# Optimization experiments

Measured on AMD Instinct MI355X. Metric: run time of the kernel, lower is better.

## Reference

```python
import jax, jax.numpy as jnp
import numpy as np

N_NODES = 100000
HIDDEN = 64
N_LAYERS = 4
N_EDGES = 800000
EPS = 1e-5  # equinox RMSNorm default


def rmsnorm(x, w):
    # per-node RMSNorm over last dim, learned scale, no bias
    inv = jax.lax.rsqrt(jnp.mean(x * x, axis=-1, keepdims=True) + EPS)
    return x * inv * w


def setup_inputs() -> dict:
    key = jax.random.key(0)
    ks = jax.random.split(key, 5)
    x = jax.random.normal(ks[0], (N_NODES, HIDDEN), dtype=jnp.float32)
    # eqx Linear weight (out,in), init ~ U(-1/sqrt(in), 1/sqrt(in)); randn*scale is fine for a baseline
    scale = 1.0 / np.sqrt(HIDDEN)
    conv_w = jax.random.normal(ks[1], (N_LAYERS, HIDDEN, HIDDEN), dtype=jnp.float32) * scale
    hid_w = jax.random.normal(ks[2], (N_LAYERS, HIDDEN, HIDDEN), dtype=jnp.float32) * scale
    conv_norm_w = jnp.ones((N_LAYERS, HIDDEN), dtype=jnp.float32)
    hid_norm_w = jnp.ones((N_LAYERS, HIDDEN), dtype=jnp.float32)
    row = jax.random.randint(ks[3], (N_EDGES,), 0, N_NODES, dtype=jnp.int32)
    col = jax.random.randint(ks[4], (N_EDGES,), 0, N_NODES, dtype=jnp.int32)
    return {"x": x, "conv_w": conv_w, "conv_norm_w": conv_norm_w,
            "hid_w": hid_w, "hid_norm_w": hid_norm_w, "row": row, "col": col}


def reference(x, conv_w, conv_norm_w, hid_w, hid_norm_w, row, col):
    n_nodes = x.shape[0]

    def step(h, params):
        cw, cnw, hw, hnw = params
        # GConvLayer: linear (no bias) -> relu -> sparse adjacency aggregation -> residual RMSNorm
        m = jax.nn.relu(h @ cw.T)                                  # [n_nodes, d]
        agg = jax.ops.segment_sum(m[col], row, num_segments=n_nodes)  # a @ m (unweighted COO)
        h = rmsnorm(h + agg, cnw)
        # HiddenLayer: linear -> relu -> residual RMSNorm
        y = jax.nn.relu(h @ hw.T)
        h = rmsnorm(h + y, hnw)
        return h, None

    x, _ = jax.lax.scan(step, x, (conv_w, conv_norm_w, hid_w, hid_norm_w))
    return x
```

## Files before the change

### kernel.cpp

```cpp
#include <hip/hip_runtime.h>
#include <hip/hip_bf16.h>

#define HIDDEN 64
#define EPS 1e-5f
#define NPB 64
#define FNPB 32
#define WST 72

typedef __attribute__((ext_vector_type(8))) short bf16x8;
typedef __attribute__((ext_vector_type(4))) float f32x4;

__device__ __forceinline__ unsigned short f2b(float x) {
    __hip_bfloat16 b = __float2bfloat16(x);
    return *(unsigned short*)&b;
}
__device__ __forceinline__ float b2f(unsigned short u) {
    unsigned int ui = (unsigned int)u << 16;
    return *(float*)&ui;
}
__device__ __forceinline__ float b2f_lo(unsigned int u) { unsigned int ui = u << 16; return *(float*)&ui; }
__device__ __forceinline__ float b2f_hi(unsigned int u) { unsigned int ui = u & 0xffff0000u; return *(float*)&ui; }
__device__ __forceinline__ unsigned int pk2(float a, float b) {
    return (unsigned int)f2b(a) | ((unsigned int)f2b(b) << 16);
}


__global__ __launch_bounds__(256) void hist_rank_kernel(const int* __restrict__ row,
                                                        int* __restrict__ cnt,
                                                        int* __restrict__ erank, int e) {
    int stride = gridDim.x * blockDim.x;
    for (int i = blockIdx.x * blockDim.x + threadIdx.x; i < e; i += stride) {
        int r = row[i];
        erank[i] = atomicAdd(&cnt[r], 1);
    }
}

__global__ __launch_bounds__(256) void block_sum_kernel(const int* __restrict__ cnt,
                                                        int* __restrict__ bsum, int n) {
    __shared__ int wsum[4];
    int tid = threadIdx.x;
    int i = blockIdx.x * 256 + tid;
    int v = (i < n) ? cnt[i] : 0;
#pragma unroll
    for (int off = 32; off > 0; off >>= 1) v += __shfl_xor(v, off, 64);
    if ((tid & 63) == 0) wsum[tid >> 6] = v;
    __syncthreads();
    if (tid == 0) bsum[blockIdx.x] = wsum[0] + wsum[1] + wsum[2] + wsum[3];
}

__global__ __launch_bounds__(256) void scan_final_kernel(const int* __restrict__ cnt,
                                                         const int* __restrict__ bsum,
                                                         int* __restrict__ row_ptr,
                                                         int n, int nb) {
    __shared__ int wred[4];
    __shared__ int wsum[4];
    __shared__ int wexcl[4];
    __shared__ int s_prev;
    __shared__ int s_tot;
    int b = blockIdx.x;
    int tid = threadIdx.x;
    int lane = tid & 63;
    int w = tid >> 6;
    int acc = 0;
    for (int j = tid; j < b; j += 256) acc += bsum[j];
#pragma unroll
    for (int off = 32; off > 0; off >>= 1) acc += __shfl_xor(acc, off, 64);
    if (lane == 0) wred[w] = acc;
    int i = b * 256 + tid;
    int v = (i < n) ? cnt[i] : 0;
    int sc = v;
#pragma unroll
    for (int off = 1; off < 64; off <<= 1) {
        int t = __shfl_up(sc, off, 64);
        if (lane >= off) sc += t;
    }
    if (lane == 63) wsum[w] = sc;
    __syncthreads();
    if (tid == 0) {
        s_prev = wred[0] + wred[1] + wred[2] + wred[3];
        int a = 0;
#pragma unroll
        for (int j = 0; j < 4; j++) { wexcl[j] = a; a += wsum[j]; }
        s_tot = a;
    }
    __syncthreads();
    if (i < n) row_ptr[i] = s_prev + wexcl[w] + (sc - v);
    if (b == nb - 1 && tid == 0) row_ptr[n] = s_prev + s_tot;
}

__global__ __launch_bounds__(256) void fill_kernel(const int* __restrict__ row,
                                                   const int* __restrict__ col,
                                                   const int* __restrict__ row_ptr,
                                                   const int* __restrict__ erank,
                                                   int* __restrict__ ecol, int e, int n) {
    int cls = blockIdx.x & 7;
    int sub = blockIdx.x >> 3;
    int nsub = gridDim.x >> 3;
    int lo = (int)(((long long)n * cls) >> 3);
    int hi = (int)(((long long)n * (cls + 1)) >> 3);
    for (int i = sub * 256 + threadIdx.x; i < e; i += nsub * 256) {
        int r = row[i];
        if (r >= lo && r < hi) {
            int pos = row_ptr[r] + erank[i];
            ecol[pos] = col[i];
        }
    }
}

__global__ __launch_bounds__(256) void wconv_kernel(const float* __restrict__ cw,
                                                    const float* __restrict__ hw,
                                                    unsigned short* __restrict__ wbt,
                                                    unsigned short* __restrict__ mA,
                                                    unsigned short* __restrict__ mB,
                                                    int L, int n) {
    int idx = blockIdx.x * blockDim.x + threadIdx.x;
    int total = 2 * L * 4096;
    if (idx < total) {
        int mat = idx >> 12;
        int rem = idx & 4095;
        const float* src = (mat < L) ? (cw + (size_t)mat * 4096) : (hw + (size_t)(mat - L) * 4096);
        wbt[idx] = f2b(src[rem]);
    } else if (idx < total + HIDDEN) {
        int k = idx - total;
        mA[(size_t)n * HIDDEN + k] = 0;
        mB[(size_t)n * HIDDEN + k] = 0;
    }
}


__device__ __forceinline__ void mfma_tile(const unsigned short* s_a,
                                          const unsigned short* s_b,
                                          int l16, int quad, int wbase, f32x4 acc[4]) {
    const unsigned short* ap = &s_a[(size_t)(wbase + l16) * WST + quad * 8];
    const unsigned short* bp = &s_b[(size_t)l16 * WST + quad * 8];
#pragma unroll
    for (int kt = 0; kt < 2; kt++) {
        bf16x8 a = *(const bf16x8*)(ap + kt * 32);
#pragma unroll
        for (int nt = 0; nt < 4; nt++) {
            bf16x8 b = *(const bf16x8*)(bp + (size_t)nt * 16 * WST + kt * 32);
            acc[nt] = __builtin_amdgcn_mfma_f32_16x16x32_bf16(a, b, acc[nt], 0, 0, 0);
        }
    }
}

__device__ __forceinline__ void load_wfrag(const unsigned short* __restrict__ w,
                                           int l16, int quad, bf16x8 wf[8]) {
    const unsigned short* wp = w + (size_t)l16 * 64 + quad * 8;
#pragma unroll
    for (int nt = 0; nt < 4; nt++) {
#pragma unroll
        for (int kt = 0; kt < 2; kt++)
            wf[nt * 2 + kt] = *(const bf16x8*)(wp + (size_t)nt * 16 * 64 + kt * 32);
    }
}

__device__ __forceinline__ void stage_wb(const unsigned short* __restrict__ wsrc,
                                         unsigned short* s_wb, int tid) {
    for (int i = tid; i < 512; i += 256) {
        int r = i >> 3, seg = i & 7;
        *(uint4*)(&s_wb[r * WST + seg * 8]) = ((const uint4*)(wsrc + r * 64))[seg];
    }
}

__device__ __forceinline__ void acc8(float* p, uint4 u) {
    p[0] += b2f_lo(u.x);
    p[1] += b2f_hi(u.x);
    p[2] += b2f_lo(u.y);
    p[3] += b2f_hi(u.y);
    p[4] += b2f_lo(u.z);
    p[5] += b2f_hi(u.z);
    p[6] += b2f_lo(u.w);
    p[7] += b2f_hi(u.w);
}


__global__ __launch_bounds__(256) void mm_relu_kernel(const float* __restrict__ h,
                                                      const unsigned short* __restrict__ wb,
                                                      __hip_bfloat16* __restrict__ m, int n) {
    __shared__ unsigned short s_hb[NPB * WST];
    __shared__ unsigned short s_wb[64 * WST];
    int tid = threadIdx.x;
    int base = blockIdx.x * NPB;
    stage_wb(wb, s_wb, tid);
    for (int i = tid; i < 512; i += 256) {
        int r = i >> 3, seg = i & 7;
        if (base + r < n) {
            const float4* hp = (const float4*)(h + (size_t)(base + r) * HIDDEN + seg * 8);
            float4 ha = hp[0], hb = hp[1];
            uint4 p;
            p.x = pk2(ha.x, ha.y);
            p.y = pk2(ha.z, ha.w);
            p.z = pk2(hb.x, hb.y);
            p.w = pk2(hb.z, hb.w);
            *(uint4*)(&s_hb[r * WST + seg * 8]) = p;
        } else {
            *(uint4*)(&s_hb[r * WST + seg * 8]) = make_uint4(0u, 0u, 0u, 0u);
        }
    }
    __syncthreads();
    int lane = tid & 63, wave = tid >> 6;
    int quad = lane >> 4, l16 = lane & 15;
    int wbase = wave * 16;
    f32x4 acc[4];
    acc[0] = (f32x4){0.f,0.f,0.f,0.f}; acc[1] = (f32x4){0.f,0.f,0.f,0.f};
    acc[2] = (f32x4){0.f,0.f,0.f,0.f}; acc[3] = (f32x4){0.f,0.f,0.f,0.f};
    mfma_tile(s_hb, s_wb, l16, quad, wbase, acc);
    unsigned short* mo = (unsigned short*)m;
#pragma unroll
    for (int r = 0; r < 4; r++) {
        int node = base + wbase + quad * 4 + r;
        if (node < n) {
#pragma unroll
            for (int nt = 0; nt < 4; nt++)
                mo[(size_t)node * HIDDEN + nt * 16 + l16] = f2b(fmaxf(acc[nt][r], 0.f));
        }
    }
}


__global__ __launch_bounds__(128, 6) void fused_layer_kernel(
        const float* hf, const __hip_bfloat16* hb_in,
        const __hip_bfloat16* __restrict__ m_in,
        const unsigned short* __restrict__ hwb,
        const unsigned short* cwb_next,
        const int* __restrict__ row_ptr, const int* __restrict__ ecol,
        const float* __restrict__ cnw, const float* __restrict__ hnw,
        float* out_f32, __hip_bfloat16* hb_new, __hip_bfloat16* m_out, int n) {
    __shared__ unsigned short s_hb[FNPB * WST];
    int tid = threadIdx.x;
    int base = blockIdx.x * FNPB;
    int lane = tid & 63, wave = tid >> 6;

    int g = lane >> 2;
    int sl = lane & 3;
    int gb = lane & ~3;
    int nl = wave * 16 + g;
    int node = base + nl;

    const unsigned short* mi = (const unsigned short*)m_in;

    uint4 q0 = make_uint4(0u, 0u, 0u, 0u);
    uint4 q1 = make_uint4(0u, 0u, 0u, 0u);
    if (node < n) {
        float p[16];
        if (hf) {
            const float4* hp = (const float4*)(hf + (size_t)node * HIDDEN + 16 * sl);
            float4 v0 = hp[0], v1 = hp[1], v2 = hp[2], v3 = hp[3];
            p[0]=v0.x;  p[1]=v0.y;  p[2]=v0.z;  p[3]=v0.w;
            p[4]=v1.x;  p[5]=v1.y;  p[6]=v1.z;  p[7]=v1.w;
            p[8]=v2.x;  p[9]=v2.y;  p[10]=v2.z; p[11]=v2.w;
            p[12]=v3.x; p[13]=v3.y; p[14]=v3.z; p[15]=v3.w;
        } else {
            const uint4* hp = (const uint4*)((const unsigned short*)hb_in + (size_t)node * HIDDEN + 16 * sl);
            uint4 u0 = hp[0], u1 = hp[1];
            p[0]=b2f_lo(u0.x);  p[1]=b2f_hi(u0.x);
            p[2]=b2f_lo(u0.y);  p[3]=b2f_hi(u0.y);
            p[4]=b2f_lo(u0.z);  p[5]=b2f_hi(u0.z);
            p[6]=b2f_lo(u0.w);  p[7]=b2f_hi(u0.w);
            p[8]=b2f_lo(u1.x);  p[9]=b2f_hi(u1.x);
            p[10]=b2f_lo(u1.y); p[11]=b2f_hi(u1.y);
            p[12]=b2f_lo(u1.z); p[13]=b2f_hi(u1.z);
            p[14]=b2f_lo(u1.w); p[15]=b2f_hi(u1.w);
        }
        int beg = row_ptr[node];
        int end = row_ptr[node + 1];
        int myc = 0;
        if (beg < end) {
            int idx = beg + sl;
            myc = ecol[idx < end ? idx : end - 1];
        }
        for (int b0 = beg; b0 < end; b0 += 4) {
            int nxt = b0 + 4;
            int nmyc = 0;
            if (nxt < end) {
                int idx = nxt + sl;
                nmyc = ecol[idx < end ? idx : end - 1];
            }
            int cnt = end - b0;
            int cj[4];
#pragma unroll
            for (int j = 0; j < 4; j++) {
                int c = __shfl(myc, gb + j, 64);
                cj[j] = (j < cnt) ? c : n;
            }
            uint4 ua[4], ub[4];
#pragma unroll
            for (int j = 0; j < 4; j++) {
                const uint4* mp = (const uint4*)(mi + (size_t)cj[j] * HIDDEN + 16 * sl);
                ua[j] = mp[0];
                ub[j] = mp[1];
            }
#pragma unroll
            for (int j = 0; j < 4; j++) {
                acc8(p, ua[j]);
                acc8(p + 8, ub[j]);
            }
            myc = nmyc;
        }
        float ss = 0.f;
#pragma unroll
        for (int k = 0; k < 16; k++) ss += p[k] * p[k];
        ss += __shfl_xor(ss, 1, 64);
        ss += __shfl_xor(ss, 2, 64);
        float inv = rsqrtf(ss * (1.0f / 64.0f) + EPS);
        const float4* cp = (const float4*)(cnw + 16 * sl);
        float4 c0 = cp[0], c1 = cp[1], c2 = cp[2], c3 = cp[3];
        q0.x = pk2(p[0]*inv*c0.x,  p[1]*inv*c0.y);
        q0.y = pk2(p[2]*inv*c0.z,  p[3]*inv*c0.w);
        q0.z = pk2(p[4]*inv*c1.x,  p[5]*inv*c1.y);
        q0.w = pk2(p[6]*inv*c1.z,  p[7]*inv*c1.w);
        q1.x = pk2(p[8]*inv*c2.x,  p[9]*inv*c2.y);
        q1.y = pk2(p[10]*inv*c2.z, p[11]*inv*c2.w);
        q1.z = pk2(p[12]*inv*c3.x, p[13]*inv*c3.y);
        q1.w = pk2(p[14]*inv*c3.z, p[15]*inv*c3.w);
    }
    *(uint4*)(&s_hb[(size_t)nl * WST + 16 * sl]) = q0;
    *(uint4*)(&s_hb[(size_t)nl * WST + 16 * sl + 8]) = q1;

    int quad = lane >> 4, l16 = lane & 15;
    int wbase = wave * 16;
    bf16x8 wfh[8];
    load_wfrag(hwb, l16, quad, wfh);
    f32x4 acc[4];
    acc[0] = (f32x4){0.f,0.f,0.f,0.f}; acc[1] = (f32x4){0.f,0.f,0.f,0.f};
    acc[2] = (f32x4){0.f,0.f,0.f,0.f}; acc[3] = (f32x4){0.f,0.f,0.f,0.f};
    {
        const unsigned short* ap = &s_hb[(size_t)(wbase + l16) * WST + quad * 8];
#pragma unroll
        for (int kt = 0; kt < 2; kt++) {
            bf16x8 a = *(const bf16x8*)(ap + kt * 32);
#pragma unroll
            for (int nt = 0; nt < 4; nt++)
                acc[nt] = __builtin_amdgcn_mfma_f32_16x16x32_bf16(a, wfh[nt * 2 + kt], acc[nt], 0, 0, 0);
        }
    }

    float hv[4][4];
    float ssq[4] = {0.f, 0.f, 0.f, 0.f};
#pragma unroll
    for (int r = 0; r < 4; r++) {
        int nr = wbase + quad * 4 + r;
#pragma unroll
        for (int nt = 0; nt < 4; nt++) {
            float hres = b2f(s_hb[(size_t)nr * WST + nt * 16 + l16]);
            float v = hres + fmaxf(acc[nt][r], 0.f);
            hv[r][nt] = v;
            ssq[r] += v * v;
        }
    }
#pragma unroll
    for (int mk = 1; mk <= 8; mk <<= 1) {
#pragma unroll
        for (int r = 0; r < 4; r++) ssq[r] += __shfl_xor(ssq[r], mk, 64);
    }
    bf16x8 wfc[8];
    if (m_out) load_wfrag(cwb_next, l16, quad, wfc);
    float nwv[4];
#pragma unroll
    for (int nt = 0; nt < 4; nt++) nwv[nt] = hnw[nt * 16 + l16];
#pragma unroll
    for (int r = 0; r < 4; r++) {
        float inv = rsqrtf(ssq[r] * (1.0f / 64.0f) + EPS);
#pragma unroll
        for (int nt = 0; nt < 4; nt++) hv[r][nt] *= inv * nwv[nt];
    }
    if (out_f32) {
#pragma unroll
        for (int r = 0; r < 4; r++) {
            int nd = base + wbase + quad * 4 + r;
            if (nd < n) {
#pragma unroll
                for (int nt = 0; nt < 4; nt++)
                    out_f32[(size_t)nd * HIDDEN + nt * 16 + l16] = hv[r][nt];
            }
        }
    }
    if (hb_new) {
        unsigned short* ho = (unsigned short*)hb_new;
#pragma unroll
        for (int r = 0; r < 4; r++) {
            int nd = base + wbase + quad * 4 + r;
            if (nd < n) {
#pragma unroll
                for (int nt = 0; nt < 4; nt++)
                    ho[(size_t)nd * HIDDEN + nt * 16 + l16] = f2b(hv[r][nt]);
            }
        }
    }

    if (!m_out) return;

#pragma unroll
    for (int r = 0; r < 4; r++) {
        int nr = wbase + quad * 4 + r;
#pragma unroll
        for (int nt = 0; nt < 4; nt++)
            s_hb[(size_t)nr * WST + nt * 16 + l16] = f2b(hv[r][nt]);
    }

    f32x4 acc2[4];
    acc2[0] = (f32x4){0.f,0.f,0.f,0.f}; acc2[1] = (f32x4){0.f,0.f,0.f,0.f};
    acc2[2] = (f32x4){0.f,0.f,0.f,0.f}; acc2[3] = (f32x4){0.f,0.f,0.f,0.f};
    {
        const unsigned short* ap = &s_hb[(size_t)(wbase + l16) * WST + quad * 8];
#pragma unroll
        for (int kt = 0; kt < 2; kt++) {
            bf16x8 a = *(const bf16x8*)(ap + kt * 32);
#pragma unroll
            for (int nt = 0; nt < 4; nt++)
                acc2[nt] = __builtin_amdgcn_mfma_f32_16x16x32_bf16(a, wfc[nt * 2 + kt], acc2[nt], 0, 0, 0);
        }
    }
    unsigned short* mo = (unsigned short*)m_out;
#pragma unroll
    for (int r = 0; r < 4; r++) {
        int nd = base + wbase + quad * 4 + r;
        if (nd < n) {
#pragma unroll
            for (int nt = 0; nt < 4; nt++)
                mo[(size_t)nd * HIDDEN + nt * 16 + l16] = f2b(fmaxf(acc2[nt][r], 0.f));
        }
    }
}


static inline size_t align_up(size_t x, size_t a) { return (x + a - 1) & ~(a - 1); }

extern "C" void kernel_launch(void* const* d_in, const int* in_sizes, int n_in,
                              void* d_out, int out_size, void* d_ws, size_t ws_size,
                              hipStream_t stream) {
    const float* x       = (const float*)d_in[0];
    const float* conv_w  = (const float*)d_in[1];
    const float* conv_nw = (const float*)d_in[2];
    const float* hid_w   = (const float*)d_in[3];
    const float* hid_nw  = (const float*)d_in[4];
    const int*   row     = (const int*)d_in[5];
    const int*   col     = (const int*)d_in[6];
    float* out = (float*)d_out;

    const int n = in_sizes[0] / HIDDEN;
    const int e = in_sizes[5];
    const int L = in_sizes[1] / 4096;

    size_t off = 0;
    char* ws = (char*)d_ws;
    __hip_bfloat16* mA = (__hip_bfloat16*)(ws + off);  off = align_up(off + (size_t)(n + 1) * HIDDEN * 2, 16);
    __hip_bfloat16* mB = (__hip_bfloat16*)(ws + off);  off = align_up(off + (size_t)(n + 1) * HIDDEN * 2, 16);
    __hip_bfloat16* hb1 = (__hip_bfloat16*)(ws + off); off = align_up(off + (size_t)n * HIDDEN * 2, 16);
    __hip_bfloat16* hb2 = (__hip_bfloat16*)(ws + off); off = align_up(off + (size_t)n * HIDDEN * 2, 16);
    unsigned short* wbt = (unsigned short*)(ws + off); off = align_up(off + (size_t)2 * L * 4096 * 2, 16);
    int* row_ptr = (int*)(ws + off);           off = align_up(off + (size_t)(n + 1) * 4, 16);
    int* cnt = (int*)(ws + off);               off = align_up(off + (size_t)n * 4, 16);
    int* bsum = (int*)(ws + off);              off = align_up(off + (size_t)1024 * 4, 16);
    int* erank = (int*)(ws + off);             off = align_up(off + (size_t)e * 4, 16);
    int* ecol = (int*)(ws + off);              off = align_up(off + (size_t)e * 4, 16);

    const int nb = (n + 255) / 256;

    hipMemsetAsync(cnt, 0, (size_t)n * 4, stream);
    hist_rank_kernel<<<1024, 256, 0, stream>>>(row, cnt, erank, e);
    block_sum_kernel<<<nb, 256, 0, stream>>>(cnt, bsum, n);
    scan_final_kernel<<<nb, 256, 0, stream>>>(cnt, bsum, row_ptr, n, nb);
    fill_kernel<<<1024, 256, 0, stream>>>(row, col, row_ptr, erank, ecol, e, n);

    wconv_kernel<<<(2 * L * 4096 + HIDDEN + 255) / 256, 256, 0, stream>>>(
        conv_w, hid_w, wbt, (unsigned short*)mA, (unsigned short*)mB, L, n);

    mm_relu_kernel<<<(n + NPB - 1) / NPB, 256, 0, stream>>>(x, wbt, mA, n);

    const int fblocks = (n + FNPB - 1) / FNPB;
    const __hip_bfloat16* mi = mA;
    __hip_bfloat16* mo = mB;
    __hip_bfloat16* hin = nullptr;
    __hip_bfloat16* hout = hb1;
    for (int l = 0; l < L; l++) {
        bool last = (l == L - 1);
        fused_layer_kernel<<<fblocks, 128, 0, stream>>>(
            (l == 0) ? x : nullptr, hin, mi,
            wbt + (size_t)(L + l) * 4096,
            last ? nullptr : (wbt + (size_t)(l + 1) * 4096),
            row_ptr, ecol,
            conv_nw + (size_t)l * HIDDEN, hid_nw + (size_t)l * HIDDEN,
            last ? out : nullptr,
            last ? nullptr : hout,
            last ? nullptr : mo, n);
        __hip_bfloat16* tmp = (__hip_bfloat16*)mi; mi = mo; mo = tmp;
        hin = hout;
        hout = (hout == hb1) ? hb2 : hb1;
    }
}
```

Baseline: 296.6 us.

## Use eight lanes per node in fused layer gather with 256-thread blocks

Each node's gather and RMSNorm is now handled by 8 lanes instead of 4. Each lane loads 16 bytes per neighbor row, and the loop processes 8 edges per iteration, so more independent memory loads are in flight. Blocks grow to 256 threads (4 waves), each wave covering 8 nodes. Each wave's 16-row MFMA tile is now half filled with zero padding, which doubles the matrix work and the wave count per node in exchange for more gather parallelism.

```diff
diff --git a/kernel.cpp b/kernel.cpp
--- a/kernel.cpp
+++ b/kernel.cpp
@@ -219,7 +219,7 @@
 }
 
 
-__global__ __launch_bounds__(128, 6) void fused_layer_kernel(
+__global__ __launch_bounds__(256, 6) void fused_layer_kernel(
         const float* hf, const __hip_bfloat16* hb_in,
         const __hip_bfloat16* __restrict__ m_in,
         const unsigned short* __restrict__ hwb,
@@ -227,41 +227,35 @@
         const int* __restrict__ row_ptr, const int* __restrict__ ecol,
         const float* __restrict__ cnw, const float* __restrict__ hnw,
         float* out_f32, __hip_bfloat16* hb_new, __hip_bfloat16* m_out, int n) {
-    __shared__ unsigned short s_hb[FNPB * WST];
+    __shared__ unsigned short s_hb[64 * WST];
     int tid = threadIdx.x;
     int base = blockIdx.x * FNPB;
     int lane = tid & 63, wave = tid >> 6;
 
-    int g = lane >> 2;
-    int sl = lane & 3;
-    int gb = lane & ~3;
+    int g = lane >> 3;
+    int sl = lane & 7;
+    int gb = lane & ~7;
     int nl = wave * 16 + g;
-    int node = base + nl;
+    int node = base + wave * 8 + g;
+
+    *(uint4*)(&s_hb[(size_t)(wave * 16 + 8 + g) * WST + 8 * sl]) = make_uint4(0u, 0u, 0u, 0u);
 
     const unsigned short* mi = (const unsigned short*)m_in;
 
     uint4 q0 = make_uint4(0u, 0u, 0u, 0u);
-    uint4 q1 = make_uint4(0u, 0u, 0u, 0u);
     if (node < n) {
-        float p[16];
+        float p[8];
         if (hf) {
-            const float4* hp = (const float4*)(hf + (size_t)node * HIDDEN + 16 * sl);
-            float4 v0 = hp[0], v1 = hp[1], v2 = hp[2], v3 = hp[3];
-            p[0]=v0.x;  p[1]=v0.y;  p[2]=v0.z;  p[3]=v0.w;
-            p[4]=v1.x;  p[5]=v1.y;  p[6]=v1.z;  p[7]=v1.w;
-            p[8]=v2.x;  p[9]=v2.y;  p[10]=v2.z; p[11]=v2.w;
-            p[12]=v3.x; p[13]=v3.y; p[14]=v3.z; p[15]=v3.w;
+            const float4* hp = (const float4*)(hf + (size_t)node * HIDDEN + 8 * sl);
+            float4 v0 = hp[0], v1 = hp[1];
+            p[0]=v0.x; p[1]=v0.y; p[2]=v0.z; p[3]=v0.w;
+            p[4]=v1.x; p[5]=v1.y; p[6]=v1.z; p[7]=v1.w;
         } else {
-            const uint4* hp = (const uint4*)((const unsigned short*)hb_in + (size_t)node * HIDDEN + 16 * sl);
-            uint4 u0 = hp[0], u1 = hp[1];
-            p[0]=b2f_lo(u0.x);  p[1]=b2f_hi(u0.x);
-            p[2]=b2f_lo(u0.y);  p[3]=b2f_hi(u0.y);
-            p[4]=b2f_lo(u0.z);  p[5]=b2f_hi(u0.z);
-            p[6]=b2f_lo(u0.w);  p[7]=b2f_hi(u0.w);
-            p[8]=b2f_lo(u1.x);  p[9]=b2f_hi(u1.x);
-            p[10]=b2f_lo(u1.y); p[11]=b2f_hi(u1.y);
-            p[12]=b2f_lo(u1.z); p[13]=b2f_hi(u1.z);
-            p[14]=b2f_lo(u1.w); p[15]=b2f_hi(u1.w);
+            uint4 u0 = *(const uint4*)((const unsigned short*)hb_in + (size_t)node * HIDDEN + 8 * sl);
+            p[0]=b2f_lo(u0.x); p[1]=b2f_hi(u0.x);
+            p[2]=b2f_lo(u0.y); p[3]=b2f_hi(u0.y);
+            p[4]=b2f_lo(u0.z); p[5]=b2f_hi(u0.z);
+            p[6]=b2f_lo(u0.w); p[7]=b2f_hi(u0.w);
         }
         int beg = row_ptr[node];
         int end = row_ptr[node + 1];
@@ -270,53 +264,44 @@
             int idx = beg + sl;
             myc = ecol[idx < end ? idx : end - 1];
         }
-        for (int b0 = beg; b0 < end; b0 += 4) {
-            int nxt = b0 + 4;
+        for (int b0 = beg; b0 < end; b0 += 8) {
+            int nxt = b0 + 8;
             int nmyc = 0;
             if (nxt < end) {
                 int idx = nxt + sl;
                 nmyc = ecol[idx < end ? idx : end - 1];
             }
             int cnt = end - b0;
-            int cj[4];
-#pragma unroll
-            for (int j = 0; j < 4; j++) {
+            int cj[8];
+#pragma unroll
+            for (int j = 0; j < 8; j++) {
                 int c = __shfl(myc, gb + j, 64);
                 cj[j] = (j < cnt) ? c : n;
             }
-            uint4 ua[4], ub[4];
-#pragma unroll
-            for (int j = 0; j < 4; j++) {
-                const uint4* mp = (const uint4*)(mi + (size_t)cj[j] * HIDDEN + 16 * sl);
-                ua[j] = mp[0];
-                ub[j] = mp[1];
-            }
-#pragma unroll
-            for (int j = 0; j < 4; j++) {
-                acc8(p, ua[j]);
-                acc8(p + 8, ub[j]);
-            }
+            uint4 u[8];
+#pragma unroll
+            for (int j = 0; j < 8; j++)
+                u[j] = *(const uint4*)(mi + (size_t)cj[j] * HIDDEN + 8 * sl);
+#pragma unroll
+            for (int j = 0; j < 8; j++)
+                acc8(p, u[j]);
             myc = nmyc;
         }
         float ss = 0.f;
 #pragma unroll
-        for (int k = 0; k < 16; k++) ss += p[k] * p[k];
+        for (int k = 0; k < 8; k++) ss += p[k] * p[k];
         ss += __shfl_xor(ss, 1, 64);
         ss += __shfl_xor(ss, 2, 64);
+        ss += __shfl_xor(ss, 4, 64);
         float inv = rsqrtf(ss * (1.0f / 64.0f) + EPS);
-        const float4* cp = (const float4*)(cnw + 16 * sl);
-        float4 c0 = cp[0], c1 = cp[1], c2 = cp[2], c3 = cp[3];
-        q0.x = pk2(p[0]*inv*c0.x,  p[1]*inv*c0.y);
-        q0.y = pk2(p[2]*inv*c0.z,  p[3]*inv*c0.w);
-        q0.z = pk2(p[4]*inv*c1.x,  p[5]*inv*c1.y);
-        q0.w = pk2(p[6]*inv*c1.z,  p[7]*inv*c1.w);
-        q1.x = pk2(p[8]*inv*c2.x,  p[9]*inv*c2.y);
-        q1.y = pk2(p[10]*inv*c2.z, p[11]*inv*c2.w);
-        q1.z = pk2(p[12]*inv*c3.x, p[13]*inv*c3.y);
-        q1.w = pk2(p[14]*inv*c3.z, p[15]*inv*c3.w);
-    }
-    *(uint4*)(&s_hb[(size_t)nl * WST + 16 * sl]) = q0;
-    *(uint4*)(&s_hb[(size_t)nl * WST + 16 * sl + 8]) = q1;
+        const float4* cp = (const float4*)(cnw + 8 * sl);
+        float4 c0 = cp[0], c1 = cp[1];
+        q0.x = pk2(p[0]*inv*c0.x, p[1]*inv*c0.y);
+        q0.y = pk2(p[2]*inv*c0.z, p[3]*inv*c0.w);
+        q0.z = pk2(p[4]*inv*c1.x, p[5]*inv*c1.y);
+        q0.w = pk2(p[6]*inv*c1.z, p[7]*inv*c1.w);
+    }
+    *(uint4*)(&s_hb[(size_t)nl * WST + 8 * sl]) = q0;
 
     int quad = lane >> 4, l16 = lane & 15;
     int wbase = wave * 16;
@@ -368,8 +353,9 @@
     if (out_f32) {
 #pragma unroll
         for (int r = 0; r < 4; r++) {
-            int nd = base + wbase + quad * 4 + r;
-            if (nd < n) {
+            int rr = quad * 4 + r;
+            int nd = base + wave * 8 + rr;
+            if (rr < 8 && nd < n) {
 #pragma unroll
                 for (int nt = 0; nt < 4; nt++)
                     out_f32[(size_t)nd * HIDDEN + nt * 16 + l16] = hv[r][nt];
@@ -380,8 +366,9 @@
         unsigned short* ho = (unsigned short*)hb_new;
 #pragma unroll
         for (int r = 0; r < 4; r++) {
-            int nd = base + wbase + quad * 4 + r;
-            if (nd < n) {
+            int rr = quad * 4 + r;
+            int nd = base + wave * 8 + rr;
+            if (rr < 8 && nd < n) {
 #pragma unroll
                 for (int nt = 0; nt < 4; nt++)
                     ho[(size_t)nd * HIDDEN + nt * 16 + l16] = f2b(hv[r][nt]);
@@ -415,8 +402,9 @@
     unsigned short* mo = (unsigned short*)m_out;
 #pragma unroll
     for (int r = 0; r < 4; r++) {
-        int nd = base + wbase + quad * 4 + r;
-        if (nd < n) {
+        int rr = quad * 4 + r;
+        int nd = base + wave * 8 + rr;
+        if (rr < 8 && nd < n) {
 #pragma unroll
             for (int nt = 0; nt < 4; nt++)
                 mo[(size_t)nd * HIDDEN + nt * 16 + l16] = f2b(fmaxf(acc2[nt][r], 0.f));
@@ -476,7 +464,7 @@
     __hip_bfloat16* hout = hb1;
     for (int l = 0; l < L; l++) {
         bool last = (l == L - 1);
-        fused_layer_kernel<<<fblocks, 128, 0, stream>>>(
+        fused_layer_kernel<<<fblocks, 256, 0, stream>>>(
             (l == 0) ? x : nullptr, hin, mi,
             wbt + (size_t)(L + l) * 4096,
             last ? nullptr : (wbt + (size_t)(l + 1) * 4096),
```

After: 360.8 us. 21.6% more time.

## Sort nodes by degree into a permutation and merge setup kernels

Applied to the files above, without the earlier changes.

Builds a per-node degree histogram (capped at 32) and a counting-sort permutation so that the fused layer kernel processes nodes grouped by similar in-degree, which reduces wave divergence in the neighbor-gather loop. It also merges the histogram and weight-conversion kernels, and the CSR fill, first matmul and permutation build, into combined launches to cut launch count. The cost is an extra perm indirection on every node load and scattered output stores, plus atomics in the setup phase.

```diff
diff --git a/kernel.cpp b/kernel.cpp
--- a/kernel.cpp
+++ b/kernel.cpp
@@ -6,6 +6,7 @@
 #define NPB 64
 #define FNPB 32
 #define WST 72
+#define NBIN 33
 
 typedef __attribute__((ext_vector_type(8))) short bf16x8;
 typedef __attribute__((ext_vector_type(4))) float f32x4;
@@ -25,32 +26,62 @@
 }
 
 
-__global__ __launch_bounds__(256) void hist_rank_kernel(const int* __restrict__ row,
-                                                        int* __restrict__ cnt,
-                                                        int* __restrict__ erank, int e) {
-    int stride = gridDim.x * blockDim.x;
-    for (int i = blockIdx.x * blockDim.x + threadIdx.x; i < e; i += stride) {
-        int r = row[i];
-        erank[i] = atomicAdd(&cnt[r], 1);
+__global__ __launch_bounds__(256) void hist_wconv_kernel(
+        const int* __restrict__ row, int* __restrict__ cnt, int* __restrict__ erank, int e,
+        const float* __restrict__ cw, const float* __restrict__ hw,
+        unsigned short* __restrict__ wbt,
+        unsigned short* __restrict__ mA, unsigned short* __restrict__ mB,
+        int L, int n) {
+    int b = blockIdx.x;
+    if (b < 1024) {
+        int stride = 1024 * 256;
+        for (int i = b * 256 + threadIdx.x; i < e; i += stride) {
+            int r = row[i];
+            erank[i] = atomicAdd(&cnt[r], 1);
+        }
+    } else {
+        int idx = (b - 1024) * 256 + threadIdx.x;
+        int total = 2 * L * 4096;
+        if (idx < total) {
+            int mat = idx >> 12;
+            int rem = idx & 4095;
+            const float* src = (mat < L) ? (cw + (size_t)mat * 4096) : (hw + (size_t)(mat - L) * 4096);
+            wbt[idx] = f2b(src[rem]);
+        } else if (idx < total + HIDDEN) {
+            int k = idx - total;
+            mA[(size_t)n * HIDDEN + k] = 0;
+            mB[(size_t)n * HIDDEN + k] = 0;
+        }
     }
 }
 
 __global__ __launch_bounds__(256) void block_sum_kernel(const int* __restrict__ cnt,
-                                                        int* __restrict__ bsum, int n) {
+                                                        int* __restrict__ bsum,
+                                                        int* __restrict__ binh, int n) {
     __shared__ int wsum[4];
+    __shared__ int lb[NBIN];
     int tid = threadIdx.x;
+    if (tid < NBIN) lb[tid] = 0;
+    __syncthreads();
     int i = blockIdx.x * 256 + tid;
     int v = (i < n) ? cnt[i] : 0;
+    if (i < n) {
+        int d = v > 32 ? 32 : v;
+        atomicAdd(&lb[d], 1);
+    }
 #pragma unroll
     for (int off = 32; off > 0; off >>= 1) v += __shfl_xor(v, off, 64);
     if ((tid & 63) == 0) wsum[tid >> 6] = v;
     __syncthreads();
     if (tid == 0) bsum[blockIdx.x] = wsum[0] + wsum[1] + wsum[2] + wsum[3];
+    if (tid < NBIN && lb[tid] > 0) atomicAdd(&binh[tid], lb[tid]);
 }
 
 __global__ __launch_bounds__(256) void scan_final_kernel(const int* __restrict__ cnt,
                                                          const int* __restrict__ bsum,
                                                          int* __restrict__ row_ptr,
+                                                         const int* __restrict__ binh,
+                                                         int* __restrict__ binb,
                                                          int n, int nb) {
     __shared__ int wred[4];
     __shared__ int wsum[4];
@@ -61,6 +92,11 @@
     int tid = threadIdx.x;
     int lane = tid & 63;
     int w = tid >> 6;
+    if (b == 0 && tid == 0) {
+        int run = 0;
+#pragma unroll 1
+        for (int j = 0; j < NBIN; j++) { binb[j] = run; run += binh[j]; }
+    }
     int acc = 0;
     for (int j = tid; j < b; j += 256) acc += bsum[j];
 #pragma unroll
@@ -86,45 +122,6 @@
     __syncthreads();
     if (i < n) row_ptr[i] = s_prev + wexcl[w] + (sc - v);
     if (b == nb - 1 && tid == 0) row_ptr[n] = s_prev + s_tot;
-}
-
-__global__ __launch_bounds__(256) void fill_kernel(const int* __restrict__ row,
-                                                   const int* __restrict__ col,
-                                                   const int* __restrict__ row_ptr,
-                                                   const int* __restrict__ erank,
-                                                   int* __restrict__ ecol, int e, int n) {
-    int cls = blockIdx.x & 7;
-    int sub = blockIdx.x >> 3;
-    int nsub = gridDim.x >> 3;
-    int lo = (int)(((long long)n * cls) >> 3);
-    int hi = (int)(((long long)n * (cls + 1)) >> 3);
-    for (int i = sub * 256 + threadIdx.x; i < e; i += nsub * 256) {
-        int r = row[i];
-        if (r >= lo && r < hi) {
-            int pos = row_ptr[r] + erank[i];
-            ecol[pos] = col[i];
-        }
-    }
-}
-
-__global__ __launch_bounds__(256) void wconv_kernel(const float* __restrict__ cw,
-                                                    const float* __restrict__ hw,
-                                                    unsigned short* __restrict__ wbt,
-                                                    unsigned short* __restrict__ mA,
-                                                    unsigned short* __restrict__ mB,
-                                                    int L, int n) {
-    int idx = blockIdx.x * blockDim.x + threadIdx.x;
-    int total = 2 * L * 4096;
-    if (idx < total) {
-        int mat = idx >> 12;
-        int rem = idx & 4095;
-        const float* src = (mat < L) ? (cw + (size_t)mat * 4096) : (hw + (size_t)(mat - L) * 4096);
-        wbt[idx] = f2b(src[rem]);
-    } else if (idx < total + HIDDEN) {
-        int k = idx - total;
-        mA[(size_t)n * HIDDEN + k] = 0;
-        mB[(size_t)n * HIDDEN + k] = 0;
-    }
 }
 
 
@@ -175,13 +172,54 @@
 }
 
 
-__global__ __launch_bounds__(256) void mm_relu_kernel(const float* __restrict__ h,
-                                                      const unsigned short* __restrict__ wb,
-                                                      __hip_bfloat16* __restrict__ m, int n) {
+__global__ __launch_bounds__(256) void fill_mm_perm_kernel(
+        const int* __restrict__ row, const int* __restrict__ col,
+        const int* __restrict__ row_ptr, const int* __restrict__ erank,
+        int* __restrict__ ecol, int e, int n,
+        const float* __restrict__ h, const unsigned short* __restrict__ wb,
+        __hip_bfloat16* __restrict__ m,
+        const int* __restrict__ cnt, int* __restrict__ binb, int* __restrict__ perm,
+        int mmblocks) {
     __shared__ unsigned short s_hb[NPB * WST];
     __shared__ unsigned short s_wb[64 * WST];
+    __shared__ int lbin[NBIN];
+    __shared__ int lbase[NBIN];
     int tid = threadIdx.x;
-    int base = blockIdx.x * NPB;
+    int bid = blockIdx.x;
+    if (bid >= mmblocks + 1024) {
+        int c = bid - (mmblocks + 1024);
+        if (tid < NBIN) lbin[tid] = 0;
+        __syncthreads();
+        int i = c * 256 + tid;
+        int d = -1, rank = 0;
+        if (i < n) {
+            int dv = cnt[i];
+            d = dv > 32 ? 32 : dv;
+            rank = atomicAdd(&lbin[d], 1);
+        }
+        __syncthreads();
+        if (tid < NBIN && lbin[tid] > 0) lbase[tid] = atomicAdd(&binb[tid], lbin[tid]);
+        __syncthreads();
+        if (d >= 0) perm[lbase[d] + rank] = i;
+        return;
+    }
+    if (bid >= mmblocks) {
+        int fb = bid - mmblocks;
+        int cls = fb & 7;
+        int sub = fb >> 3;
+        int nsub = 128;
+        int lo = (int)(((long long)n * cls) >> 3);
+        int hi = (int)(((long long)n * (cls + 1)) >> 3);
+        for (int i = sub * 256 + tid; i < e; i += nsub * 256) {
+            int r = row[i];
+            if (r >= lo && r < hi) {
+                int pos = row_ptr[r] + erank[i];
+                ecol[pos] = col[i];
+            }
+        }
+        return;
+    }
+    int base = bid * NPB;
     stage_wb(wb, s_wb, tid);
     for (int i = tid; i < 512; i += 256) {
         int r = i >> 3, seg = i & 7;
@@ -225,6 +263,7 @@
         const unsigned short* __restrict__ hwb,
         const unsigned short* cwb_next,
         const int* __restrict__ row_ptr, const int* __restrict__ ecol,
+        const int* __restrict__ perm,
         const float* __restrict__ cnw, const float* __restrict__ hnw,
         float* out_f32, __hip_bfloat16* hb_new, __hip_bfloat16* m_out, int n) {
     __shared__ unsigned short s_hb[FNPB * WST];
@@ -236,13 +275,14 @@
     int sl = lane & 3;
     int gb = lane & ~3;
     int nl = wave * 16 + g;
-    int node = base + nl;
+    int pidx = base + nl;
+    int node = (pidx < n) ? perm[pidx] : -1;
 
     const unsigned short* mi = (const unsigned short*)m_in;
 
     uint4 q0 = make_uint4(0u, 0u, 0u, 0u);
     uint4 q1 = make_uint4(0u, 0u, 0u, 0u);
-    if (node < n) {
+    if (node >= 0) {
         float p[16];
         if (hf) {
             const float4* hp = (const float4*)(hf + (size_t)node * HIDDEN + 16 * sl);
@@ -277,12 +317,12 @@
                 int idx = nxt + sl;
                 nmyc = ecol[idx < end ? idx : end - 1];
             }
-            int cnt = end - b0;
+            int cnt4 = end - b0;
             int cj[4];
 #pragma unroll
             for (int j = 0; j < 4; j++) {
                 int c = __shfl(myc, gb + j, 64);
-                cj[j] = (j < cnt) ? c : n;
+                cj[j] = (j < cnt4) ? c : n;
             }
             uint4 ua[4], ub[4];
 #pragma unroll
@@ -336,6 +376,13 @@
         }
     }
 
+    int pr[4];
+#pragma unroll
+    for (int r = 0; r < 4; r++) {
+        int pidx_r = base + wbase + quad * 4 + r;
+        pr[r] = (pidx_r < n) ? perm[pidx_r] : -1;
+    }
+
     float hv[4][4];
     float ssq[4] = {0.f, 0.f, 0.f, 0.f};
 #pragma unroll
@@ -368,11 +415,10 @@
     if (out_f32) {
 #pragma unroll
         for (int r = 0; r < 4; r++) {
-            int nd = base + wbase + quad * 4 + r;
-            if (nd < n) {
+            if (pr[r] >= 0) {
 #pragma unroll
                 for (int nt = 0; nt < 4; nt++)
-                    out_f32[(size_t)nd * HIDDEN + nt * 16 + l16] = hv[r][nt];
+                    out_f32[(size_t)pr[r] * HIDDEN + nt * 16 + l16] = hv[r][nt];
             }
         }
     }
@@ -380,11 +426,10 @@
         unsigned short* ho = (unsigned short*)hb_new;
 #pragma unroll
         for (int r = 0; r < 4; r++) {
-            int nd = base + wbase + quad * 4 + r;
-            if (nd < n) {
+            if (pr[r] >= 0) {
 #pragma unroll
                 for (int nt = 0; nt < 4; nt++)
-                    ho[(size_t)nd * HIDDEN + nt * 16 + l16] = f2b(hv[r][nt]);
+                    ho[(size_t)pr[r] * HIDDEN + nt * 16 + l16] = f2b(hv[r][nt]);
             }
         }
     }
@@ -415,11 +460,10 @@
     unsigned short* mo = (unsigned short*)m_out;
 #pragma unroll
     for (int r = 0; r < 4; r++) {
-        int nd = base + wbase + quad * 4 + r;
-        if (nd < n) {
+        if (pr[r] >= 0) {
 #pragma unroll
             for (int nt = 0; nt < 4; nt++)
-                mo[(size_t)nd * HIDDEN + nt * 16 + l16] = f2b(fmaxf(acc2[nt][r], 0.f));
+                mo[(size_t)pr[r] * HIDDEN + nt * 16 + l16] = f2b(fmaxf(acc2[nt][r], 0.f));
         }
     }
 }
@@ -451,23 +495,28 @@
     __hip_bfloat16* hb2 = (__hip_bfloat16*)(ws + off); off = align_up(off + (size_t)n * HIDDEN * 2, 16);
     unsigned short* wbt = (unsigned short*)(ws + off); off = align_up(off + (size_t)2 * L * 4096 * 2, 16);
     int* row_ptr = (int*)(ws + off);           off = align_up(off + (size_t)(n + 1) * 4, 16);
-    int* cnt = (int*)(ws + off);               off = align_up(off + (size_t)n * 4, 16);
+    int* cnt = (int*)(ws + off);
+    int* binh = cnt + n;
+    int* binb = binh + 64;
+    off = align_up(off + (size_t)(n + 128) * 4, 16);
+    int* perm = (int*)(ws + off);              off = align_up(off + (size_t)n * 4, 16);
     int* bsum = (int*)(ws + off);              off = align_up(off + (size_t)1024 * 4, 16);
     int* erank = (int*)(ws + off);             off = align_up(off + (size_t)e * 4, 16);
     int* ecol = (int*)(ws + off);              off = align_up(off + (size_t)e * 4, 16);
 
     const int nb = (n + 255) / 256;
-
-    hipMemsetAsync(cnt, 0, (size_t)n * 4, stream);
-    hist_rank_kernel<<<1024, 256, 0, stream>>>(row, cnt, erank, e);
-    block_sum_kernel<<<nb, 256, 0, stream>>>(cnt, bsum, n);
-    scan_final_kernel<<<nb, 256, 0, stream>>>(cnt, bsum, row_ptr, n, nb);
-    fill_kernel<<<1024, 256, 0, stream>>>(row, col, row_ptr, erank, ecol, e, n);
-
-    wconv_kernel<<<(2 * L * 4096 + HIDDEN + 255) / 256, 256, 0, stream>>>(
-        conv_w, hid_w, wbt, (unsigned short*)mA, (unsigned short*)mB, L, n);
-
-    mm_relu_kernel<<<(n + NPB - 1) / NPB, 256, 0, stream>>>(x, wbt, mA, n);
+    const int wconv_blocks = (2 * L * 4096 + HIDDEN + 255) / 256;
+    const int mmblocks = (n + NPB - 1) / NPB;
+
+    hipMemsetAsync(cnt, 0, (size_t)(n + 64) * 4, stream);
+    hist_wconv_kernel<<<1024 + wconv_blocks, 256, 0, stream>>>(
+        row, cnt, erank, e, conv_w, hid_w, wbt,
+        (unsigned short*)mA, (unsigned short*)mB, L, n);
+    block_sum_kernel<<<nb, 256, 0, stream>>>(cnt, bsum, binh, n);
+    scan_final_kernel<<<nb, 256, 0, stream>>>(cnt, bsum, row_ptr, binh, binb, n, nb);
+    fill_mm_perm_kernel<<<mmblocks + 1024 + nb, 256, 0, stream>>>(
+        row, col, row_ptr, erank, ecol, e, n, x, wbt, mA,
+        cnt, binb, perm, mmblocks);
 
     const int fblocks = (n + FNPB - 1) / FNPB;
     const __hip_bfloat16* mi = mA;
@@ -480,7 +529,7 @@
             (l == 0) ? x : nullptr, hin, mi,
             wbt + (size_t)(L + l) * 4096,
             last ? nullptr : (wbt + (size_t)(l + 1) * 4096),
-            row_ptr, ecol,
+            row_ptr, ecol, perm,
             conv_nw + (size_t)l * HIDDEN, hid_nw + (size_t)l * HIDDEN,
             last ? out : nullptr,
             last ? nullptr : hout,
```

Result: no change. 291.8 us (-1.6%).
